# Kernel optimization log

Measured on AMD Instinct MI355X. Metric: run time of the kernel, lower is better.

The kernel has to match this reference:

```python
import jax, jax.numpy as jnp
import numpy as np

N, D, K, H, G = 200000, 256, 128, 4, 1024  # nodes, emb_dim, hidden, heads, graphs


def setup_inputs() -> dict:
    key = jax.random.key(0)
    k0, k1, k2, k3 = jax.random.split(key, 4)
    node_features = jax.random.normal(k0, (N, D), jnp.float32)
    segment_ids = jnp.sort(jax.random.randint(k1, (N,), 0, G)).astype(jnp.int32)
    W1 = jax.random.normal(k2, (H, D, K), jnp.float32) / np.float32(np.sqrt(D))
    b1 = jnp.zeros((H, K), jnp.float32)
    W2 = jax.random.normal(k3, (H, K), jnp.float32) / np.float32(np.sqrt(K))
    b2 = jnp.zeros((H,), jnp.float32)
    return {"node_features": node_features, "segment_ids": segment_ids,
            "num_graphs": G, "W1": W1, "b1": b1, "W2": W2, "b2": b2}


def _segment_softmax(scores, seg, num_segments):
    # scores: [N, H]; numerically-stable softmax within each graph segment, per head
    m = jax.ops.segment_max(scores, seg, num_segments=num_segments)  # [G, H]
    e = jnp.exp(scores - m[seg])
    s = jax.ops.segment_sum(e, seg, num_segments=num_segments)  # [G, H]
    return e / s[seg]


def reference(node_features, segment_ids, num_graphs, W1, b1, W2, b2):
    # Per-head MLP score for all heads at once: [N, H]
    h = jax.nn.relu(jnp.einsum('nd,hdk->nhk', node_features, W1) + b1)
    scores = jnp.einsum('nhk,hk->nh', h, W2) + b2
    # dgl.softmax_nodes per head == segment softmax over graph ids
    attn = _segment_softmax(scores, segment_ids, num_graphs)  # [N, H]
    # combine_type == 'mean': mean_h segment_sum(attn_h * x)
    # == segment_sum(mean_h(attn_h) * x) since the sum is linear in attn.
    avg_attn = attn.mean(axis=1)  # [N]
    weighted = avg_attn[:, None] * node_features  # [N, D]
    return jax.ops.segment_sum(weighted, segment_ids, num_segments=num_graphs)  # [G, D]
```

## Files before the change

### kernel.cpp

```cpp
#include <hip/hip_runtime.h>
#include <hip/hip_bf16.h>

typedef unsigned short u16;
typedef __attribute__((ext_vector_type(8))) __bf16 bf16x8;
typedef __attribute__((ext_vector_type(8))) u16 u16x8;
typedef __attribute__((ext_vector_type(4))) float f32x4;

__device__ __forceinline__ u16 f2bf(float f) {
    unsigned u = __float_as_uint(f);
    u += 0x7fffu + ((u >> 16) & 1u);
    return (u16)(u >> 16);
}

__device__ __forceinline__ void gl_lds16(const void* g, void* l) {
    __builtin_amdgcn_global_load_lds(
        (const __attribute__((address_space(1))) void*)g,
        (__attribute__((address_space(3))) void*)l, 16, 0, 0);
}

__global__ __launch_bounds__(256) void transpose_w1(const float* __restrict__ W1,
                                                    u16* __restrict__ W1T) {
    __shared__ u16 tile[64][132];
    const int t = threadIdx.x;
    const int h = blockIdx.x >> 2;
    const int dt = blockIdx.x & 3;
#pragma unroll
    for (int j = 0; j < 8; ++j) {
        int idx = j * 256 + t;
        int r = idx >> 5;
        int kq = idx & 31;
        float4 v = *reinterpret_cast<const float4*>(
            W1 + ((size_t)h * 256 + dt * 64 + r) * 128 + kq * 4);
        ushort4 o;
        o.x = f2bf(v.x); o.y = f2bf(v.y); o.z = f2bf(v.z); o.w = f2bf(v.w);
        *reinterpret_cast<ushort4*>(&tile[r][kq * 4]) = o;
    }
    __syncthreads();
#pragma unroll
    for (int j = 0; j < 4; ++j) {
        int idx = j * 256 + t;
        int k = idx >> 3;
        int c8 = idx & 7;
        u16x8 o;
#pragma unroll
        for (int e = 0; e < 8; ++e) o[e] = tile[c8 * 8 + e][k];
        *reinterpret_cast<u16x8*>(W1T + ((size_t)h * 128 + k) * 256 + dt * 64 + c8 * 8) = o;
    }
}

__global__ __launch_bounds__(256, 2) void score_kernel(
        const float* __restrict__ x, const u16* __restrict__ W1T,
        const float* __restrict__ b1, const float* __restrict__ W2,
        const float* __restrict__ b2, float* __restrict__ scores, int N) {
    __shared__ u16 xb[16384];
    __shared__ u16 sA[16384];

    const int t = threadIdx.x;
    const int wave = t >> 6;
    const int lane = t & 63;
    const int l15 = lane & 15;
    const int quad = lane >> 4;
    const int n0 = blockIdx.x * 64;

    {
        const int nrow = wave * 16 + (lane >> 2);
        const int koff = (lane & 3) * 8;
        int nn = n0 + nrow; if (nn >= N) nn = N - 1;
        const float* src = x + (size_t)nn * 256 + koff;
        float4 v[16];
#pragma unroll
        for (int i = 0; i < 8; ++i) {
            v[2 * i]     = *reinterpret_cast<const float4*>(src + i * 32);
            v[2 * i + 1] = *reinterpret_cast<const float4*>(src + i * 32 + 4);
        }
#pragma unroll
        for (int i = 0; i < 8; ++i) {
            u16x8 o;
            o[0] = f2bf(v[2*i].x);   o[1] = f2bf(v[2*i].y);
            o[2] = f2bf(v[2*i].z);   o[3] = f2bf(v[2*i].w);
            o[4] = f2bf(v[2*i+1].x); o[5] = f2bf(v[2*i+1].y);
            o[6] = f2bf(v[2*i+1].z); o[7] = f2bf(v[2*i+1].w);
            *reinterpret_cast<u16x8*>(&xb[(i * 256 + t) * 8]) = o;
        }
    }

    const int arr = (lane >> 2);
    const int akc = (lane & 3) * 8;
    auto stageA = [&](int ks) {
        const int k0 = ks * 32;
#pragma unroll
        for (int j = 0; j < 8; ++j) {
            int fr = wave * 8 + j;
            const u16* g = W1T + (size_t)(fr * 16 + arr) * 256 + k0 + akc;
            gl_lds16(g, &sA[(size_t)fr * 512]);
        }
    };

    f32x4 acc[8][4] = {};
    stageA(0);
    __syncthreads();

    for (int ks = 0; ks < 8; ++ks) {
        bf16x8 a[8], b[4];
#pragma unroll
        for (int fr = 0; fr < 8; ++fr)
            a[fr] = *reinterpret_cast<const bf16x8*>(
                &sA[((wave * 8 + fr) * 64 + l15 * 4 + quad) * 8]);
#pragma unroll
        for (int nf = 0; nf < 4; ++nf)
            b[nf] = *reinterpret_cast<const bf16x8*>(
                &xb[((ks * 4 + nf) * 64 + l15 * 4 + quad) * 8]);
        __syncthreads();
        if (ks < 7) stageA(ks + 1);
#pragma unroll
        for (int fr = 0; fr < 8; ++fr)
#pragma unroll
            for (int nf = 0; nf < 4; ++nf)
                acc[fr][nf] = __builtin_amdgcn_mfma_f32_16x16x32_bf16(
                    a[fr], b[nf], acc[fr][nf], 0, 0, 0);
        __syncthreads();
    }

    const int h = wave;
    float4 b1v[8], w2v[8];
#pragma unroll
    for (int fr = 0; fr < 8; ++fr) {
        int rb = h * 128 + fr * 16 + quad * 4;
        b1v[fr] = *reinterpret_cast<const float4*>(b1 + rb);
        w2v[fr] = *reinterpret_cast<const float4*>(W2 + rb);
    }
    const float b2v = b2[h];
#pragma unroll
    for (int nf = 0; nf < 4; ++nf) {
        float p = 0.f;
#pragma unroll
        for (int fr = 0; fr < 8; ++fr) {
            f32x4 c = acc[fr][nf];
            p += fmaxf(c[0] + b1v[fr].x, 0.f) * w2v[fr].x
               + fmaxf(c[1] + b1v[fr].y, 0.f) * w2v[fr].y
               + fmaxf(c[2] + b1v[fr].z, 0.f) * w2v[fr].z
               + fmaxf(c[3] + b1v[fr].w, 0.f) * w2v[fr].w;
        }
        p += __shfl_xor(p, 16, 64);
        p += __shfl_xor(p, 32, 64);
        int n = n0 + nf * 16 + lane;
        if (lane < 16 && n < N)
            scores[(size_t)n * 4 + h] = p + b2v;
    }
}

__device__ __forceinline__ int lower_bound(const int* __restrict__ a, int n, int v) {
    int lo = 0, hi = n;
    while (lo < hi) {
        int mid = (lo + hi) >> 1;
        if (a[mid] < v) lo = mid + 1; else hi = mid;
    }
    return lo;
}

__global__ __launch_bounds__(256) void segstat_kernel(
        const float4* __restrict__ scores4, const int* __restrict__ seg,
        float4* __restrict__ mOut, float4* __restrict__ isOut, int N) {
    __shared__ float4 redm[4];
    __shared__ float4 reds[4];
    const int g = blockIdx.x;
    const int t = threadIdx.x;
    const int start = lower_bound(seg, N, g);
    const int end = lower_bound(seg, N, g + 1);

    float4 mx = make_float4(-3.4e38f, -3.4e38f, -3.4e38f, -3.4e38f);
    for (int i = start + t; i < end; i += 256) {
        float4 s = scores4[i];
        mx.x = fmaxf(mx.x, s.x); mx.y = fmaxf(mx.y, s.y);
        mx.z = fmaxf(mx.z, s.z); mx.w = fmaxf(mx.w, s.w);
    }
#pragma unroll
    for (int off = 1; off < 64; off <<= 1) {
        mx.x = fmaxf(mx.x, __shfl_xor(mx.x, off, 64));
        mx.y = fmaxf(mx.y, __shfl_xor(mx.y, off, 64));
        mx.z = fmaxf(mx.z, __shfl_xor(mx.z, off, 64));
        mx.w = fmaxf(mx.w, __shfl_xor(mx.w, off, 64));
    }
    if ((t & 63) == 0) redm[t >> 6] = mx;
    __syncthreads();
    mx = redm[0];
#pragma unroll
    for (int w = 1; w < 4; ++w) {
        mx.x = fmaxf(mx.x, redm[w].x); mx.y = fmaxf(mx.y, redm[w].y);
        mx.z = fmaxf(mx.z, redm[w].z); mx.w = fmaxf(mx.w, redm[w].w);
    }

    float4 sm = make_float4(0.f, 0.f, 0.f, 0.f);
    for (int i = start + t; i < end; i += 256) {
        float4 s = scores4[i];
        sm.x += expf(s.x - mx.x); sm.y += expf(s.y - mx.y);
        sm.z += expf(s.z - mx.z); sm.w += expf(s.w - mx.w);
    }
#pragma unroll
    for (int off = 1; off < 64; off <<= 1) {
        sm.x += __shfl_xor(sm.x, off, 64);
        sm.y += __shfl_xor(sm.y, off, 64);
        sm.z += __shfl_xor(sm.z, off, 64);
        sm.w += __shfl_xor(sm.w, off, 64);
    }
    if ((t & 63) == 0) reds[t >> 6] = sm;
    __syncthreads();
    if (t == 0) {
        float4 tot = reds[0];
        for (int w = 1; w < 4; ++w) {
            tot.x += reds[w].x; tot.y += reds[w].y;
            tot.z += reds[w].z; tot.w += reds[w].w;
        }
        bool nonempty = end > start;
        float4 m_out = nonempty ? mx : make_float4(0.f, 0.f, 0.f, 0.f);
        float4 is;
        is.x = (nonempty && tot.x > 0.f) ? 1.f / tot.x : 0.f;
        is.y = (nonempty && tot.y > 0.f) ? 1.f / tot.y : 0.f;
        is.z = (nonempty && tot.z > 0.f) ? 1.f / tot.z : 0.f;
        is.w = (nonempty && tot.w > 0.f) ? 1.f / tot.w : 0.f;
        mOut[g] = m_out;
        isOut[g] = is;
    }
}

__global__ __launch_bounds__(256) void wsum_kernel(
        const float* __restrict__ x, const float4* __restrict__ scores4,
        const int* __restrict__ seg, const float4* __restrict__ mArr,
        const float4* __restrict__ isArr, float* __restrict__ out, int N) {
    __shared__ float wl[64];
    __shared__ int gl[64];
    __shared__ unsigned long long bmask_s;
    const int t = threadIdx.x;
    const int n0 = blockIdx.x * 64;
    const int cnt = min(64, N - n0);

    if (t < 64) {
        int g = -1;
        float w = 0.f;
        bool bnd = false;
        if (t < cnt) {
            int n = n0 + t;
            g = seg[n];
            float4 s = scores4[n];
            float4 m = mArr[g];
            float4 is = isArr[g];
            w = 0.25f * (expf(s.x - m.x) * is.x + expf(s.y - m.y) * is.y +
                         expf(s.z - m.z) * is.z + expf(s.w - m.w) * is.w);
            bnd = (t > 0) && (g != seg[n - 1]);
        }
        wl[t] = w;
        gl[t] = g;
        unsigned long long bm = __ballot(bnd);
        if (t == 0) bmask_s = bm;
    }
    __syncthreads();
    const unsigned long long bmask = bmask_s;

    int rs = 0;
    while (rs < cnt) {
        unsigned long long mm = (rs < 63) ? (bmask & ((~0ULL) << (rs + 1))) : 0ULL;
        int re = mm ? (__ffsll((long long)mm) - 1) : cnt;
        if (re > cnt) re = cnt;
        float acc = 0.f;
        int i = rs;
        for (; i + 8 <= re; i += 8) {
            float xv[8];
#pragma unroll
            for (int j = 0; j < 8; ++j)
                xv[j] = x[(size_t)(n0 + i + j) * 256 + t];
#pragma unroll
            for (int j = 0; j < 8; ++j) acc += wl[i + j] * xv[j];
        }
        for (; i < re; ++i) acc += wl[i] * x[(size_t)(n0 + i) * 256 + t];
        atomicAdd(&out[(size_t)gl[rs] * 256 + t], acc);
        rs = re;
    }
}

extern "C" void kernel_launch(void* const* d_in, const int* in_sizes, int n_in,
                              void* d_out, int out_size, void* d_ws, size_t ws_size,
                              hipStream_t stream) {
    const float* x  = (const float*)d_in[0];
    const int* seg  = (const int*)d_in[1];
    const float* W1 = (const float*)d_in[3];
    const float* b1 = (const float*)d_in[4];
    const float* W2 = (const float*)d_in[5];
    const float* b2 = (const float*)d_in[6];
    float* out = (float*)d_out;

    const int N = in_sizes[0] / 256;
    const int G = 1024;

    char* ws = (char*)d_ws;
    float* scores = (float*)ws;
    u16* W1T      = (u16*)(ws + (size_t)N * 16);
    float* mArr   = (float*)(ws + (size_t)N * 16 + 262144);
    float* isArr  = mArr + (size_t)G * 4;

    hipMemsetAsync(d_out, 0, (size_t)G * 256 * sizeof(float), stream);
    transpose_w1<<<16, 256, 0, stream>>>(W1, W1T);
    score_kernel<<<(N + 63) / 64, 256, 0, stream>>>(x, W1T, b1, W2, b2, scores, N);
    segstat_kernel<<<G, 256, 0, stream>>>((const float4*)scores, seg,
                                          (float4*)mArr, (float4*)isArr, N);
    wsum_kernel<<<(N + 63) / 64, 256, 0, stream>>>(x, (const float4*)scores, seg,
                                                   (const float4*)mArr,
                                                   (const float4*)isArr, out, N);
}
```

Before: 383.7 us.

## Pre-swizzle W1 into MFMA fragment order and load A directly to registers

The W1 transpose kernel now writes bf16 weights in the exact per-lane MFMA fragment layout. The score kernel loads A fragments straight from global memory into double-buffered registers instead of staging them through LDS with global_load_lds, which removes the per-k-step __syncthreads barriers and the sA buffer. The x tile load is rewritten for coalesced full-row float4 reads scattered into the fragment-ordered LDS layout. The trade-off is more register pressure from two A buffers and direct global (L2-resident) weight reads by every block.

```diff
diff --git a/kernel.cpp b/kernel.cpp
--- a/kernel.cpp
+++ b/kernel.cpp
@@ -12,14 +12,8 @@
     return (u16)(u >> 16);
 }
 
-__device__ __forceinline__ void gl_lds16(const void* g, void* l) {
-    __builtin_amdgcn_global_load_lds(
-        (const __attribute__((address_space(1))) void*)g,
-        (__attribute__((address_space(3))) void*)l, 16, 0, 0);
-}
-
 __global__ __launch_bounds__(256) void transpose_w1(const float* __restrict__ W1,
-                                                    u16* __restrict__ W1T) {
+                                                    u16* __restrict__ W1A) {
     __shared__ u16 tile[64][132];
     const int t = threadIdx.x;
     const int h = blockIdx.x >> 2;
@@ -44,16 +38,17 @@
         u16x8 o;
 #pragma unroll
         for (int e = 0; e < 8; ++e) o[e] = tile[c8 * 8 + e][k];
-        *reinterpret_cast<u16x8*>(W1T + ((size_t)h * 128 + k) * 256 + dt * 64 + c8 * 8) = o;
+        size_t ua = ((size_t)(h * 64 + (k >> 4) * 8 + dt * 2 + (c8 >> 2))) * 512
+                  + (size_t)(c8 & 3) * 128 + (size_t)(k & 15) * 8;
+        *reinterpret_cast<u16x8*>(W1A + ua) = o;
     }
 }
 
 __global__ __launch_bounds__(256, 2) void score_kernel(
-        const float* __restrict__ x, const u16* __restrict__ W1T,
+        const float* __restrict__ x, const u16* __restrict__ W1A,
         const float* __restrict__ b1, const float* __restrict__ W2,
         const float* __restrict__ b2, float* __restrict__ scores, int N) {
     __shared__ u16 xb[16384];
-    __shared__ u16 sA[16384];
 
     const int t = threadIdx.x;
     const int wave = t >> 6;
@@ -62,63 +57,58 @@
     const int quad = lane >> 4;
     const int n0 = blockIdx.x * 64;
 
-    {
-        const int nrow = wave * 16 + (lane >> 2);
-        const int koff = (lane & 3) * 8;
-        int nn = n0 + nrow; if (nn >= N) nn = N - 1;
-        const float* src = x + (size_t)nn * 256 + koff;
-        float4 v[16];
+#pragma unroll
+    for (int rnd = 0; rnd < 2; ++rnd) {
+        float4 v[8];
 #pragma unroll
         for (int i = 0; i < 8; ++i) {
-            v[2 * i]     = *reinterpret_cast<const float4*>(src + i * 32);
-            v[2 * i + 1] = *reinterpret_cast<const float4*>(src + i * 32 + 4);
+            int f = (rnd * 8 + i) * 256 + t;
+            int n = f >> 6, dq = f & 63;
+            int nn = n0 + n; if (nn >= N) nn = N - 1;
+            v[i] = *reinterpret_cast<const float4*>(x + (size_t)nn * 256 + dq * 4);
         }
 #pragma unroll
         for (int i = 0; i < 8; ++i) {
-            u16x8 o;
-            o[0] = f2bf(v[2*i].x);   o[1] = f2bf(v[2*i].y);
-            o[2] = f2bf(v[2*i].z);   o[3] = f2bf(v[2*i].w);
-            o[4] = f2bf(v[2*i+1].x); o[5] = f2bf(v[2*i+1].y);
-            o[6] = f2bf(v[2*i+1].z); o[7] = f2bf(v[2*i+1].w);
-            *reinterpret_cast<u16x8*>(&xb[(i * 256 + t) * 8]) = o;
-        }
-    }
-
-    const int arr = (lane >> 2);
-    const int akc = (lane & 3) * 8;
-    auto stageA = [&](int ks) {
-        const int k0 = ks * 32;
-#pragma unroll
-        for (int j = 0; j < 8; ++j) {
-            int fr = wave * 8 + j;
-            const u16* g = W1T + (size_t)(fr * 16 + arr) * 256 + k0 + akc;
-            gl_lds16(g, &sA[(size_t)fr * 512]);
-        }
-    };
-
+            int f = (rnd * 8 + i) * 256 + t;
+            int n = f >> 6, dq = f & 63;
+            int ks = dq >> 3, qd = (dq >> 1) & 3, j0 = (dq & 1) * 4;
+            int nf = n >> 4, lr = n & 15;
+            ushort4 o;
+            o.x = f2bf(v[i].x); o.y = f2bf(v[i].y);
+            o.z = f2bf(v[i].z); o.w = f2bf(v[i].w);
+            *reinterpret_cast<ushort4*>(
+                &xb[((ks * 4 + nf) * 64 + qd * 16 + lr) * 8 + j0]) = o;
+        }
+    }
+    __syncthreads();
+
+    const u16* Abase = W1A + (size_t)(wave * 64) * 512 + (size_t)lane * 8;
     f32x4 acc[8][4] = {};
-    stageA(0);
-    __syncthreads();
-
+    bf16x8 a[2][8];
+#pragma unroll
+    for (int rf = 0; rf < 8; ++rf)
+        a[0][rf] = *reinterpret_cast<const bf16x8*>(Abase + (rf * 8 + 0) * 512);
+
+#pragma unroll
     for (int ks = 0; ks < 8; ++ks) {
-        bf16x8 a[8], b[4];
-#pragma unroll
-        for (int fr = 0; fr < 8; ++fr)
-            a[fr] = *reinterpret_cast<const bf16x8*>(
-                &sA[((wave * 8 + fr) * 64 + l15 * 4 + quad) * 8]);
+        const int cur = ks & 1;
+        bf16x8 b[4];
 #pragma unroll
         for (int nf = 0; nf < 4; ++nf)
             b[nf] = *reinterpret_cast<const bf16x8*>(
-                &xb[((ks * 4 + nf) * 64 + l15 * 4 + quad) * 8]);
-        __syncthreads();
-        if (ks < 7) stageA(ks + 1);
-#pragma unroll
-        for (int fr = 0; fr < 8; ++fr)
+                &xb[((ks * 4 + nf) * 64 + lane) * 8]);
+        if (ks < 7) {
+#pragma unroll
+            for (int rf = 0; rf < 8; ++rf)
+                a[cur ^ 1][rf] = *reinterpret_cast<const bf16x8*>(
+                    Abase + (rf * 8 + ks + 1) * 512);
+        }
+#pragma unroll
+        for (int rf = 0; rf < 8; ++rf)
 #pragma unroll
             for (int nf = 0; nf < 4; ++nf)
-                acc[fr][nf] = __builtin_amdgcn_mfma_f32_16x16x32_bf16(
-                    a[fr], b[nf], acc[fr][nf], 0, 0, 0);
-        __syncthreads();
+                acc[rf][nf] = __builtin_amdgcn_mfma_f32_16x16x32_bf16(
+                    a[cur][rf], b[nf], acc[rf][nf], 0, 0, 0);
     }
 
     const int h = wave;
@@ -293,13 +283,13 @@
 
     char* ws = (char*)d_ws;
     float* scores = (float*)ws;
-    u16* W1T      = (u16*)(ws + (size_t)N * 16);
+    u16* W1A      = (u16*)(ws + (size_t)N * 16);
     float* mArr   = (float*)(ws + (size_t)N * 16 + 262144);
     float* isArr  = mArr + (size_t)G * 4;
 
     hipMemsetAsync(d_out, 0, (size_t)G * 256 * sizeof(float), stream);
-    transpose_w1<<<16, 256, 0, stream>>>(W1, W1T);
-    score_kernel<<<(N + 63) / 64, 256, 0, stream>>>(x, W1T, b1, W2, b2, scores, N);
+    transpose_w1<<<16, 256, 0, stream>>>(W1, W1A);
+    score_kernel<<<(N + 63) / 64, 256, 0, stream>>>(x, W1A, b1, W2, b2, scores, N);
     segstat_kernel<<<G, 256, 0, stream>>>((const float4*)scores, seg,
                                           (float4*)mArr, (float4*)isArr, N);
     wsum_kernel<<<(N + 63) / 64, 256, 0, stream>>>(x, (const float4*)scores, seg,
```

After: 405.9 us. +5.8%, slower.
